# Optimization experiments

Hardware: AMD Instinct MI355X
Metric: run time of the kernel (lower is better)

Reference implementation:

```python
import jax, jax.numpy as jnp
import numpy as np

DIM = 768
HEADS = 12
HEAD_DIM = DIM // HEADS
SCALE = HEAD_DIM ** -0.5


def setup_inputs() -> dict:
    key = jax.random.key(0)
    ks = jax.random.split(key, 5)
    x = jax.random.normal(ks[0], (2, 4096, DIM), dtype=jnp.float32)
    # torch nn.Linear params: weight [out, in], bias [out]
    qkv_w = jax.random.normal(ks[1], (3 * DIM, DIM), dtype=jnp.float32) * (DIM ** -0.5)
    qkv_b = jax.random.normal(ks[2], (3 * DIM,), dtype=jnp.float32) * 0.02
    proj_w = jax.random.normal(ks[3], (DIM, DIM), dtype=jnp.float32) * (DIM ** -0.5)
    proj_b = jax.random.normal(ks[4], (DIM,), dtype=jnp.float32) * 0.02
    return {"x": x, "qkv_w": qkv_w, "qkv_b": qkv_b, "proj_w": proj_w, "proj_b": proj_b}


def reference(x, qkv_w, qkv_b, proj_w, proj_b):
    b, n, c = x.shape
    qkv = x @ qkv_w.T + qkv_b                      # [b, n, 3c]
    qkv = qkv.reshape(b, n, 3, HEADS, HEAD_DIM)
    qkv = jnp.transpose(qkv, (2, 0, 3, 1, 4))      # [3, b, h, n, d]
    q, k, v = qkv[0], qkv[1], qkv[2]
    attn = jax.nn.softmax(jnp.einsum('bhqd,bhkd->bhqk', q, k) * SCALE, axis=-1)
    out = jnp.einsum('bhqk,bhkd->bhqd', attn, v)   # [b, h, n, d]
    out = jnp.transpose(out, (0, 2, 1, 3)).reshape(b, n, c)
    return out @ proj_w.T + proj_b
```

## Files before the change

### kernel.cpp

```cpp
#include <hip/hip_runtime.h>
#include <stdint.h>

#define SEQ   4096
#define NDIM  768
#define HD    64
#define NH    12
#define NBH   24
#define MTOT  8192

#define PSTR 72

typedef short s8v __attribute__((ext_vector_type(8)));
typedef float f4v __attribute__((ext_vector_type(4)));
typedef float f16x __attribute__((ext_vector_type(16)));
typedef unsigned short u16;
typedef u16 u16x4 __attribute__((ext_vector_type(4)));
typedef uint32_t u32x4v __attribute__((ext_vector_type(4)));
typedef int i32x2 __attribute__((ext_vector_type(2)));

#define C1 0.18033688011112042f

__device__ __forceinline__ u16 f2bf(float f) {
  union { float f; uint32_t u; } cv; cv.f = f;
  const uint32_t u = cv.u;
  return (u16)((u + 0x7fffu + ((u >> 16) & 1u)) >> 16);
}
__device__ __forceinline__ float ex2(float x) { return __builtin_amdgcn_exp2f(x); }

__device__ __forceinline__ uint32_t cvtpk_bf16(float lo, float hi) {
  uint32_t r;
  asm("v_cvt_pk_bf16_f32 %0, %1, %2" : "=v"(r) : "v"(lo), "v"(hi));
  return r;
}
__device__ __forceinline__ void pl32swap(uint32_t& a, uint32_t& b) {
  i32x2 r = __builtin_amdgcn_permlane32_swap((int)a, (int)b, false, false);
  a = (uint32_t)r.x; b = (uint32_t)r.y;
}
__device__ __forceinline__ void gload_lds16(const void* g, void* l) {
  __builtin_amdgcn_global_load_lds(
      (const __attribute__((address_space(1))) uint32_t*)g,
      (__attribute__((address_space(3))) uint32_t*)l, 16, 0, 0);
}

__global__ __launch_bounds__(256) void cvt3_kernel(
    const float* __restrict__ a, u16* __restrict__ da, int na4,
    const float* __restrict__ b, u16* __restrict__ db, int nb4,
    const float* __restrict__ c, u16* __restrict__ dc, int nc4) {
  int i = blockIdx.x * 256 + threadIdx.x;
  const float* s; u16* d;
  if (i < na4)             { s = a; d = da; }
  else if (i < na4 + nb4)  { s = b; d = db; i -= na4; }
  else if (i < na4 + nb4 + nc4) { s = c; d = dc; i -= na4 + nb4; }
  else return;
  const float4 f = ((const float4*)s)[i];
  u16x4 r;
  r[0] = f2bf(f.x); r[1] = f2bf(f.y); r[2] = f2bf(f.z); r[3] = f2bf(f.w);
  ((u16x4*)d)[i] = r;
}

__global__ __launch_bounds__(256) void gemm_qkv(const u16* __restrict__ A,
    const u16* __restrict__ B, const float* __restrict__ bias,
    u16* __restrict__ qg, u16* __restrict__ kg, u16* __restrict__ vtg) {
  __shared__ __align__(16) u16 at[128 * 32];
  __shared__ __align__(16) u16 bt[128 * 32];
  const int tid  = threadIdx.x;
  const int lane = tid & 63;
  const int w    = tid >> 6;
  const int quad = lane >> 4;
  const int col  = lane & 15;
  const int m0 = blockIdx.y * 128;
  const int n0 = blockIdx.x * 128;
  const int srow = tid >> 2;
  const int schk = ((tid & 3) ^ (srow & 3)) * 8;
  const int wm = (w >> 1) * 64;
  const int wn = (w & 1) * 64;
  const int xq = (quad ^ (col & 3)) * 8;

  const f4v fz = {0.f, 0.f, 0.f, 0.f};
  f4v acc[4][4];
#pragma unroll
  for (int i = 0; i < 4; i++)
#pragma unroll
    for (int j = 0; j < 4; j++) acc[i][j] = fz;

  const u16* ga0 = A + (size_t)(m0 + srow) * NDIM + schk;
  const u16* ga1 = A + (size_t)(m0 + 64 + srow) * NDIM + schk;
  const u16* gb0 = B + (size_t)(n0 + srow) * NDIM + schk;
  const u16* gb1 = B + (size_t)(n0 + 64 + srow) * NDIM + schk;
  u16* const la = at + (size_t)w * 512;
  u16* const lb = bt + (size_t)w * 512;

  for (int k0 = 0; k0 < NDIM; k0 += 32) {
    __syncthreads();
    gload_lds16(ga0 + k0, la);
    gload_lds16(ga1 + k0, la + 2048);
    gload_lds16(gb0 + k0, lb);
    gload_lds16(gb1 + k0, lb + 2048);
    __syncthreads();
    s8v af[4], bf[4];
#pragma unroll
    for (int i = 0; i < 4; i++)
      af[i] = *(const s8v*)(at + (wm + i * 16 + col) * 32 + xq);
#pragma unroll
    for (int j = 0; j < 4; j++)
      bf[j] = *(const s8v*)(bt + (wn + j * 16 + col) * 32 + xq);
#pragma unroll
    for (int i = 0; i < 4; i++)
#pragma unroll
      for (int j = 0; j < 4; j++)
        acc[i][j] = __builtin_amdgcn_mfma_f32_16x16x32_bf16(af[i], bf[j], acc[i][j], 0, 0, 0);
  }

  const int wmg = m0 + wm;
  const int wng = n0 + wn;
  const int s = n0 / NDIM;
#pragma unroll
  for (int j = 0; j < 4; j++) {
    const int c = wng + j * 16 + col;
    const float bv = bias[c];
    const int r = c - s * NDIM;
    const int h = r >> 6;
    const int d = r & 63;
#pragma unroll
    for (int i = 0; i < 4; i++) {
      const int mb = wmg + i * 16 + quad * 4;
      const int bb = mb >> 12;
      const int n  = mb & 4095;
      const size_t hb = (size_t)(bb * NH + h);
      const f4v v = acc[i][j];
      if (s == 2) {
        u16x4 pk;
#pragma unroll
        for (int rg = 0; rg < 4; rg++) pk[rg] = f2bf(v[rg] + bv);
        *(u16x4*)(vtg + (hb * HD + d) * SEQ + n) = pk;
      } else if (s == 0) {
#pragma unroll
        for (int rg = 0; rg < 4; rg++)
          qg[(hb * SEQ + (size_t)(n + rg)) * HD + d] = f2bf((v[rg] + bv) * C1);
      } else {
#pragma unroll
        for (int rg = 0; rg < 4; rg++)
          kg[(hb * SEQ + (size_t)(n + rg)) * HD + d] = f2bf(v[rg] + bv);
      }
    }
  }
}

__global__ __launch_bounds__(256, 3) void attn_kernel(const u16* __restrict__ qg,
    const u16* __restrict__ kg, const u16* __restrict__ vtg, u16* __restrict__ og) {
  __shared__ __align__(16) u16 kls[2][64 * PSTR];
  __shared__ __align__(16) u16 vls[2][64 * PSTR];
  __shared__ float lws[4][32];

  const int tid  = threadIdx.x;
  const int lane = tid & 63;
  const int w    = tid >> 6;
  const int hi   = lane >> 5;
  const int c    = lane & 31;
  const int blk = blockIdx.x;
  const int bh  = blk % NBH;
  const int q0  = (blk / NBH) * 128;
  const size_t gbase = (size_t)bh * (SEQ * HD);
  const int wq = w * 32;

  s8v qf[4];
#pragma unroll
  for (int s = 0; s < 4; s++)
    qf[s] = *(const s8v*)(qg + gbase + (size_t)(q0 + wq + c) * HD + s * 16 + hi * 8);

  f16x o0, o1;
#pragma unroll
  for (int e = 0; e < 16; e++) { o0[e] = 0.f; o1[e] = 0.f; }
  float l0 = 0.f, l1 = 0.f, l2 = 0.f, l3 = 0.f;

  const int srow8 = tid >> 3;
  const int sch8  = (tid & 7) * 8;
  const u16* kp = kg  + gbase + (size_t)srow8 * HD  + sch8;
  const u16* vp = vtg + gbase + (size_t)srow8 * SEQ;

  s8v kr0 = *(const s8v*)(kp);
  s8v kr1 = *(const s8v*)(kp + (size_t)32 * HD);
  s8v vr0 = *(const s8v*)(vp + sch8);
  s8v vr1 = *(const s8v*)(vp + (size_t)32 * SEQ + sch8);
  *(s8v*)(kls[0] + srow8 * PSTR + sch8) = kr0;
  *(s8v*)(kls[0] + (32 + srow8) * PSTR + sch8) = kr1;
  *(s8v*)(vls[0] + srow8 * PSTR + sch8) = vr0;
  *(s8v*)(vls[0] + (32 + srow8) * PSTR + sch8) = vr1;

  for (int kb = 0; kb < SEQ; kb += 64) {
    const int cur = (kb >> 6) & 1;
    const u16* kt_ = kls[cur];
    const u16* vt_ = vls[cur];
    __syncthreads();

    if (kb + 64 < SEQ) {
      kr0 = *(const s8v*)(kp + (size_t)(kb + 64) * HD);
      kr1 = *(const s8v*)(kp + (size_t)(kb + 96) * HD);
      vr0 = *(const s8v*)(vp + kb + 64 + sch8);
      vr1 = *(const s8v*)(vp + (size_t)32 * SEQ + kb + 64 + sch8);
    }

    f16x st0, st1;
#pragma unroll
    for (int e = 0; e < 16; e++) { st0[e] = 0.f; st1[e] = 0.f; }
    __builtin_amdgcn_s_setprio(1);
#pragma unroll
    for (int s = 0; s < 4; s++) {
      const s8v k0 = *(const s8v*)(kt_ + c * PSTR + s * 16 + hi * 8);
      const s8v k1 = *(const s8v*)(kt_ + (32 + c) * PSTR + s * 16 + hi * 8);
      st0 = __builtin_amdgcn_mfma_f32_32x32x16_bf16(k0, qf[s], st0, 0, 0, 0);
      st1 = __builtin_amdgcn_mfma_f32_32x32x16_bf16(k1, qf[s], st1, 0, 0, 0);
    }
    __builtin_amdgcn_s_setprio(0);

    s8v pa0, pa1, pa2, pa3;
    {
      float p[16];
#pragma unroll
      for (int e = 0; e < 16; e++) p[e] = ex2(st0[e]);
      l0 += p[0] + p[4] + p[8]  + p[12];
      l1 += p[1] + p[5] + p[9]  + p[13];
      l2 += p[2] + p[6] + p[10] + p[14];
      l3 += p[3] + p[7] + p[11] + p[15];
      uint32_t k0 = cvtpk_bf16(p[0],  p[1]);
      uint32_t k1 = cvtpk_bf16(p[2],  p[3]);
      uint32_t k2 = cvtpk_bf16(p[4],  p[5]);
      uint32_t k3 = cvtpk_bf16(p[6],  p[7]);
      uint32_t k4 = cvtpk_bf16(p[8],  p[9]);
      uint32_t k5 = cvtpk_bf16(p[10], p[11]);
      uint32_t k6 = cvtpk_bf16(p[12], p[13]);
      uint32_t k7 = cvtpk_bf16(p[14], p[15]);
      pl32swap(k0, k2); pl32swap(k1, k3);
      pl32swap(k4, k6); pl32swap(k5, k7);
      u32x4v wA = {k0, k1, k2, k3};
      u32x4v wB = {k4, k5, k6, k7};
      pa0 = __builtin_bit_cast(s8v, wA);
      pa1 = __builtin_bit_cast(s8v, wB);
    }

    __builtin_amdgcn_s_setprio(1);
    {
      const s8v v00 = *(const s8v*)(vt_ + c * PSTR + hi * 8);
      const s8v v01 = *(const s8v*)(vt_ + (32 + c) * PSTR + hi * 8);
      const s8v v10 = *(const s8v*)(vt_ + c * PSTR + 16 + hi * 8);
      const s8v v11 = *(const s8v*)(vt_ + (32 + c) * PSTR + 16 + hi * 8);
      o0 = __builtin_amdgcn_mfma_f32_32x32x16_bf16(pa0, v00, o0, 0, 0, 0);
      o1 = __builtin_amdgcn_mfma_f32_32x32x16_bf16(pa0, v01, o1, 0, 0, 0);
      o0 = __builtin_amdgcn_mfma_f32_32x32x16_bf16(pa1, v10, o0, 0, 0, 0);
      o1 = __builtin_amdgcn_mfma_f32_32x32x16_bf16(pa1, v11, o1, 0, 0, 0);
    }
    __builtin_amdgcn_s_setprio(0);

    {
      float p[16];
#pragma unroll
      for (int e = 0; e < 16; e++) p[e] = ex2(st1[e]);
      l0 += p[0] + p[4] + p[8]  + p[12];
      l1 += p[1] + p[5] + p[9]  + p[13];
      l2 += p[2] + p[6] + p[10] + p[14];
      l3 += p[3] + p[7] + p[11] + p[15];
      uint32_t k0 = cvtpk_bf16(p[0],  p[1]);
      uint32_t k1 = cvtpk_bf16(p[2],  p[3]);
      uint32_t k2 = cvtpk_bf16(p[4],  p[5]);
      uint32_t k3 = cvtpk_bf16(p[6],  p[7]);
      uint32_t k4 = cvtpk_bf16(p[8],  p[9]);
      uint32_t k5 = cvtpk_bf16(p[10], p[11]);
      uint32_t k6 = cvtpk_bf16(p[12], p[13]);
      uint32_t k7 = cvtpk_bf16(p[14], p[15]);
      pl32swap(k0, k2); pl32swap(k1, k3);
      pl32swap(k4, k6); pl32swap(k5, k7);
      u32x4v wA = {k0, k1, k2, k3};
      u32x4v wB = {k4, k5, k6, k7};
      pa2 = __builtin_bit_cast(s8v, wA);
      pa3 = __builtin_bit_cast(s8v, wB);
    }

    if (kb + 64 < SEQ) {
      u16* kn = (u16*)kls[cur ^ 1];
      u16* vn = (u16*)vls[cur ^ 1];
      *(s8v*)(kn + srow8 * PSTR + sch8) = kr0;
      *(s8v*)(kn + (32 + srow8) * PSTR + sch8) = kr1;
      *(s8v*)(vn + srow8 * PSTR + sch8) = vr0;
      *(s8v*)(vn + (32 + srow8) * PSTR + sch8) = vr1;
    }

    __builtin_amdgcn_s_setprio(1);
    {
      const s8v v20 = *(const s8v*)(vt_ + c * PSTR + 32 + hi * 8);
      const s8v v21 = *(const s8v*)(vt_ + (32 + c) * PSTR + 32 + hi * 8);
      const s8v v30 = *(const s8v*)(vt_ + c * PSTR + 48 + hi * 8);
      const s8v v31 = *(const s8v*)(vt_ + (32 + c) * PSTR + 48 + hi * 8);
      o0 = __builtin_amdgcn_mfma_f32_32x32x16_bf16(pa2, v20, o0, 0, 0, 0);
      o1 = __builtin_amdgcn_mfma_f32_32x32x16_bf16(pa2, v21, o1, 0, 0, 0);
      o0 = __builtin_amdgcn_mfma_f32_32x32x16_bf16(pa3, v30, o0, 0, 0, 0);
      o1 = __builtin_amdgcn_mfma_f32_32x32x16_bf16(pa3, v31, o1, 0, 0, 0);
    }
    __builtin_amdgcn_s_setprio(0);
  }

  float lt = l0 + l1 + l2 + l3;
  lt += __shfl_xor(lt, 32);
  const float inv = 1.0f / lt;
  if (hi == 0) lws[w][c] = inv;

  const int b = bh / NH;
  const int h = bh % NH;
  u16* obase = og + (size_t)(b * SEQ + q0 + wq) * NDIM + h * HD + c;
#pragma unroll
  for (int r = 0; r < 16; r++) {
    const int row = (r & 3) + 8 * (r >> 2) + 4 * hi;
    const float invr = lws[w][row];
    u16* rp = obase + (size_t)row * NDIM;
    rp[0]  = f2bf(o0[r] * invr);
    rp[32] = f2bf(o1[r] * invr);
  }
}

__global__ __launch_bounds__(256) void gemm_proj(const u16* __restrict__ A,
    const u16* __restrict__ B, const float* __restrict__ bias, float* __restrict__ out) {
  __shared__ __align__(16) u16 at[128 * 32];
  __shared__ __align__(16) u16 bt[128 * 32];
  const int tid  = threadIdx.x;
  const int lane = tid & 63;
  const int w    = tid >> 6;
  const int quad = lane >> 4;
  const int col  = lane & 15;
  const int m0 = blockIdx.y * 128;
  const int n0 = blockIdx.x * 128;
  const int srow = tid >> 2;
  const int schk = ((tid & 3) ^ (srow & 3)) * 8;
  const int wm = (w >> 1) * 64;
  const int wn = (w & 1) * 64;
  const int xq = (quad ^ (col & 3)) * 8;

  const f4v fz = {0.f, 0.f, 0.f, 0.f};
  f4v acc[4][4];
#pragma unroll
  for (int i = 0; i < 4; i++)
#pragma unroll
    for (int j = 0; j < 4; j++) acc[i][j] = fz;

  const u16* ga0 = A + (size_t)(m0 + srow) * NDIM + schk;
  const u16* ga1 = A + (size_t)(m0 + 64 + srow) * NDIM + schk;
  const u16* gb0 = B + (size_t)(n0 + srow) * NDIM + schk;
  const u16* gb1 = B + (size_t)(n0 + 64 + srow) * NDIM + schk;
  u16* const la = at + (size_t)w * 512;
  u16* const lb = bt + (size_t)w * 512;

  for (int k0 = 0; k0 < NDIM; k0 += 32) {
    __syncthreads();
    gload_lds16(ga0 + k0, la);
    gload_lds16(ga1 + k0, la + 2048);
    gload_lds16(gb0 + k0, lb);
    gload_lds16(gb1 + k0, lb + 2048);
    __syncthreads();
    s8v af[4], bf[4];
#pragma unroll
    for (int i = 0; i < 4; i++)
      af[i] = *(const s8v*)(at + (wm + i * 16 + col) * 32 + xq);
#pragma unroll
    for (int j = 0; j < 4; j++)
      bf[j] = *(const s8v*)(bt + (wn + j * 16 + col) * 32 + xq);
#pragma unroll
    for (int i = 0; i < 4; i++)
#pragma unroll
      for (int j = 0; j < 4; j++)
        acc[i][j] = __builtin_amdgcn_mfma_f32_16x16x32_bf16(af[i], bf[j], acc[i][j], 0, 0, 0);
  }

  const int wmg = m0 + wm;
  const int wng = n0 + wn;
#pragma unroll
  for (int j = 0; j < 4; j++) {
    const int c = wng + j * 16 + col;
    const float bv = bias[c];
#pragma unroll
    for (int i = 0; i < 4; i++) {
#pragma unroll
      for (int rg = 0; rg < 4; rg++)
        out[(size_t)(wmg + i * 16 + quad * 4 + rg) * NDIM + c] = acc[i][j][rg] + bv;
    }
  }
}

extern "C" void kernel_launch(void* const* d_in, const int* in_sizes, int n_in,
                              void* d_out, int out_size, void* d_ws, size_t ws_size,
                              hipStream_t stream) {
  const float* x      = (const float*)d_in[0];
  const float* qkv_w  = (const float*)d_in[1];
  const float* qkv_b  = (const float*)d_in[2];
  const float* proj_w = (const float*)d_in[3];
  const float* proj_b = (const float*)d_in[4];
  float* out = (float*)d_out;

  u16* ws   = (u16*)d_ws;
  u16* x_bf = ws;
  u16* wq   = x_bf + (size_t)MTOT * NDIM;
  u16* wp   = wq + (size_t)3 * NDIM * NDIM;
  u16* q_bf = wp + (size_t)NDIM * NDIM;
  u16* k_bf = q_bf + (size_t)NBH * SEQ * HD;
  u16* vt   = k_bf + (size_t)NBH * SEQ * HD;
  u16* a_bf = vt + (size_t)NBH * SEQ * HD;

  const int nx = MTOT * NDIM / 4, nw1 = 3 * NDIM * NDIM / 4, nw2 = NDIM * NDIM / 4;
  const int ntot = nx + nw1 + nw2;
  cvt3_kernel<<<(ntot + 255) / 256, 256, 0, stream>>>(x, x_bf, nx, qkv_w, wq, nw1,
                                                      proj_w, wp, nw2);

  gemm_qkv<<<dim3(18, 64), 256, 0, stream>>>(x_bf, wq, qkv_b, q_bf, k_bf, vt);
  attn_kernel<<<768, 256, 0, stream>>>(q_bf, k_bf, vt, a_bf);
  gemm_proj<<<dim3(6, 64), 256, 0, stream>>>(a_bf, wp, proj_b, out);
}
```

Before: 278.8 us.

## Split attention key tile across wave pairs with swizzled LDS and direct loads

Restructures the attention kernel so each pair of waves owns 64 query rows and each wave in the pair handles half of every 64-key tile. The two partial outputs and row sums are then combined through shared memory at the end. The padded K/V shared tiles are replaced by an XOR-swizzled layout filled by direct global-to-LDS loads, removing the register staging and explicit shared-memory stores. V fragments are reused across two query sub-tiles, and the occupancy hint drops from 3 to 2 blocks. The costs are more accumulator registers per wave and an extra cross-wave reduction at the end.

```diff
diff --git a/kernel.cpp b/kernel.cpp
--- a/kernel.cpp
+++ b/kernel.cpp
@@ -7,8 +7,6 @@
 #define NH    12
 #define NBH   24
 #define MTOT  8192
-
-#define PSTR 72
 
 typedef short s8v __attribute__((ext_vector_type(8)));
 typedef float f4v __attribute__((ext_vector_type(4)));
@@ -146,82 +144,100 @@
   }
 }
 
-__global__ __launch_bounds__(256, 3) void attn_kernel(const u16* __restrict__ qg,
+__global__ __launch_bounds__(256, 2) void attn_kernel(const u16* __restrict__ qg,
     const u16* __restrict__ kg, const u16* __restrict__ vtg, u16* __restrict__ og) {
-  __shared__ __align__(16) u16 kls[2][64 * PSTR];
-  __shared__ __align__(16) u16 vls[2][64 * PSTR];
-  __shared__ float lws[4][32];
+  __shared__ __align__(16) u16 smem[2][2][4096];
+  __shared__ float lred[2][64];
 
   const int tid  = threadIdx.x;
   const int lane = tid & 63;
   const int w    = tid >> 6;
   const int hi   = lane >> 5;
   const int c    = lane & 31;
+  const int kth  = w & 1;
+  const int pair = w >> 1;
   const int blk = blockIdx.x;
   const int bh  = blk % NBH;
   const int q0  = (blk / NBH) * 128;
   const size_t gbase = (size_t)bh * (SEQ * HD);
-  const int wq = w * 32;
-
-  s8v qf[4];
-#pragma unroll
-  for (int s = 0; s < 4; s++)
-    qf[s] = *(const s8v*)(qg + gbase + (size_t)(q0 + wq + c) * HD + s * 16 + hi * 8);
-
-  f16x o0, o1;
-#pragma unroll
-  for (int e = 0; e < 16; e++) { o0[e] = 0.f; o1[e] = 0.f; }
-  float l0 = 0.f, l1 = 0.f, l2 = 0.f, l3 = 0.f;
-
-  const int srow8 = tid >> 3;
-  const int sch8  = (tid & 7) * 8;
-  const u16* kp = kg  + gbase + (size_t)srow8 * HD  + sch8;
-  const u16* vp = vtg + gbase + (size_t)srow8 * SEQ;
-
-  s8v kr0 = *(const s8v*)(kp);
-  s8v kr1 = *(const s8v*)(kp + (size_t)32 * HD);
-  s8v vr0 = *(const s8v*)(vp + sch8);
-  s8v vr1 = *(const s8v*)(vp + (size_t)32 * SEQ + sch8);
-  *(s8v*)(kls[0] + srow8 * PSTR + sch8) = kr0;
-  *(s8v*)(kls[0] + (32 + srow8) * PSTR + sch8) = kr1;
-  *(s8v*)(vls[0] + srow8 * PSTR + sch8) = vr0;
-  *(s8v*)(vls[0] + (32 + srow8) * PSTR + sch8) = vr1;
+  const int qw = pair * 64;
+
+  s8v qfA[4], qfB[4];
+#pragma unroll
+  for (int s = 0; s < 4; s++) {
+    qfA[s] = *(const s8v*)(qg + gbase + (size_t)(q0 + qw + c) * HD + s * 16 + hi * 8);
+    qfB[s] = *(const s8v*)(qg + gbase + (size_t)(q0 + qw + 32 + c) * HD + s * 16 + hi * 8);
+  }
+
+  f16x zacc;
+#pragma unroll
+  for (int e = 0; e < 16; e++) zacc[e] = 0.f;
+  f16x o00 = zacc, o01 = zacc, o10 = zacc, o11 = zacc;
+  float l0a = 0.f, l1a = 0.f, l2a = 0.f, l3a = 0.f;
+  float l0b = 0.f, l1b = 0.f, l2b = 0.f, l3b = 0.f;
+
+  const int lrow  = lane >> 3;
+  const int lslot = (lane & 7) ^ lrow;
+  const u16* kgl0 = kg  + gbase + (size_t)(w * 16 + lrow) * HD  + lslot * 8;
+  const u16* kgl1 = kgl0 + (size_t)8 * HD;
+  const u16* vgl0 = vtg + gbase + (size_t)(w * 16 + lrow) * SEQ + lslot * 8;
+  const u16* vgl1 = vgl0 + (size_t)8 * SEQ;
+
+  {
+    u16* kd = (u16*)smem[0][0] + w * 1024;
+    u16* vd = (u16*)smem[0][1] + w * 1024;
+    gload_lds16(kgl0, kd);
+    gload_lds16(kgl1, kd + 512);
+    gload_lds16(vgl0, vd);
+    gload_lds16(vgl1, vd + 512);
+  }
+
+  const int kbase = kth * 2048 + c * 64;
+  const int c7 = c & 7;
 
   for (int kb = 0; kb < SEQ; kb += 64) {
     const int cur = (kb >> 6) & 1;
-    const u16* kt_ = kls[cur];
-    const u16* vt_ = vls[cur];
+    const u16* kb_ = smem[cur][0];
+    const u16* vb_ = smem[cur][1];
     __syncthreads();
 
     if (kb + 64 < SEQ) {
-      kr0 = *(const s8v*)(kp + (size_t)(kb + 64) * HD);
-      kr1 = *(const s8v*)(kp + (size_t)(kb + 96) * HD);
-      vr0 = *(const s8v*)(vp + kb + 64 + sch8);
-      vr1 = *(const s8v*)(vp + (size_t)32 * SEQ + kb + 64 + sch8);
-    }
-
-    f16x st0, st1;
-#pragma unroll
-    for (int e = 0; e < 16; e++) { st0[e] = 0.f; st1[e] = 0.f; }
+      const int nb = cur ^ 1;
+      u16* kd = (u16*)smem[nb][0] + w * 1024;
+      u16* vd = (u16*)smem[nb][1] + w * 1024;
+      gload_lds16(kgl0 + (size_t)(kb + 64) * HD, kd);
+      gload_lds16(kgl1 + (size_t)(kb + 64) * HD, kd + 512);
+      gload_lds16(vgl0 + (kb + 64), vd);
+      gload_lds16(vgl1 + (kb + 64), vd + 512);
+    }
+
     __builtin_amdgcn_s_setprio(1);
-#pragma unroll
-    for (int s = 0; s < 4; s++) {
-      const s8v k0 = *(const s8v*)(kt_ + c * PSTR + s * 16 + hi * 8);
-      const s8v k1 = *(const s8v*)(kt_ + (32 + c) * PSTR + s * 16 + hi * 8);
-      st0 = __builtin_amdgcn_mfma_f32_32x32x16_bf16(k0, qf[s], st0, 0, 0, 0);
-      st1 = __builtin_amdgcn_mfma_f32_32x32x16_bf16(k1, qf[s], st1, 0, 0, 0);
+    f16x sA, sB;
+    {
+      const s8v kf0 = *(const s8v*)(kb_ + kbase + ((((0 * 2 + hi)) ^ c7) << 3));
+      sA = __builtin_amdgcn_mfma_f32_32x32x16_bf16(kf0, qfA[0], zacc, 0, 0, 0);
+      sB = __builtin_amdgcn_mfma_f32_32x32x16_bf16(kf0, qfB[0], zacc, 0, 0, 0);
+      const s8v kf1 = *(const s8v*)(kb_ + kbase + ((((1 * 2 + hi)) ^ c7) << 3));
+      sA = __builtin_amdgcn_mfma_f32_32x32x16_bf16(kf1, qfA[1], sA, 0, 0, 0);
+      sB = __builtin_amdgcn_mfma_f32_32x32x16_bf16(kf1, qfB[1], sB, 0, 0, 0);
+      const s8v kf2 = *(const s8v*)(kb_ + kbase + ((((2 * 2 + hi)) ^ c7) << 3));
+      sA = __builtin_amdgcn_mfma_f32_32x32x16_bf16(kf2, qfA[2], sA, 0, 0, 0);
+      sB = __builtin_amdgcn_mfma_f32_32x32x16_bf16(kf2, qfB[2], sB, 0, 0, 0);
+      const s8v kf3 = *(const s8v*)(kb_ + kbase + ((((3 * 2 + hi)) ^ c7) << 3));
+      sA = __builtin_amdgcn_mfma_f32_32x32x16_bf16(kf3, qfA[3], sA, 0, 0, 0);
+      sB = __builtin_amdgcn_mfma_f32_32x32x16_bf16(kf3, qfB[3], sB, 0, 0, 0);
     }
     __builtin_amdgcn_s_setprio(0);
 
-    s8v pa0, pa1, pa2, pa3;
+    s8v pa00, pa01, pa10, pa11;
     {
       float p[16];
 #pragma unroll
-      for (int e = 0; e < 16; e++) p[e] = ex2(st0[e]);
-      l0 += p[0] + p[4] + p[8]  + p[12];
-      l1 += p[1] + p[5] + p[9]  + p[13];
-      l2 += p[2] + p[6] + p[10] + p[14];
-      l3 += p[3] + p[7] + p[11] + p[15];
+      for (int e = 0; e < 16; e++) p[e] = ex2(sA[e]);
+      l0a += p[0] + p[4] + p[8]  + p[12];
+      l1a += p[1] + p[5] + p[9]  + p[13];
+      l2a += p[2] + p[6] + p[10] + p[14];
+      l3a += p[3] + p[7] + p[11] + p[15];
       uint32_t k0 = cvtpk_bf16(p[0],  p[1]);
       uint32_t k1 = cvtpk_bf16(p[2],  p[3]);
       uint32_t k2 = cvtpk_bf16(p[4],  p[5]);
@@ -234,31 +250,32 @@
       pl32swap(k4, k6); pl32swap(k5, k7);
       u32x4v wA = {k0, k1, k2, k3};
       u32x4v wB = {k4, k5, k6, k7};
-      pa0 = __builtin_bit_cast(s8v, wA);
-      pa1 = __builtin_bit_cast(s8v, wB);
-    }
-
+      pa00 = __builtin_bit_cast(s8v, wA);
+      pa01 = __builtin_bit_cast(s8v, wB);
+    }
+
+    s8v vf0, vf1, vf2, vf3;
     __builtin_amdgcn_s_setprio(1);
     {
-      const s8v v00 = *(const s8v*)(vt_ + c * PSTR + hi * 8);
-      const s8v v01 = *(const s8v*)(vt_ + (32 + c) * PSTR + hi * 8);
-      const s8v v10 = *(const s8v*)(vt_ + c * PSTR + 16 + hi * 8);
-      const s8v v11 = *(const s8v*)(vt_ + (32 + c) * PSTR + 16 + hi * 8);
-      o0 = __builtin_amdgcn_mfma_f32_32x32x16_bf16(pa0, v00, o0, 0, 0, 0);
-      o1 = __builtin_amdgcn_mfma_f32_32x32x16_bf16(pa0, v01, o1, 0, 0, 0);
-      o0 = __builtin_amdgcn_mfma_f32_32x32x16_bf16(pa1, v10, o0, 0, 0, 0);
-      o1 = __builtin_amdgcn_mfma_f32_32x32x16_bf16(pa1, v11, o1, 0, 0, 0);
+      vf0 = *(const s8v*)(vb_ + 0 * 2048 + c * 64 + (((kth * 4 + 0 + hi) ^ c7) << 3));
+      vf1 = *(const s8v*)(vb_ + 1 * 2048 + c * 64 + (((kth * 4 + 0 + hi) ^ c7) << 3));
+      vf2 = *(const s8v*)(vb_ + 0 * 2048 + c * 64 + (((kth * 4 + 2 + hi) ^ c7) << 3));
+      vf3 = *(const s8v*)(vb_ + 1 * 2048 + c * 64 + (((kth * 4 + 2 + hi) ^ c7) << 3));
+      o00 = __builtin_amdgcn_mfma_f32_32x32x16_bf16(pa00, vf0, o00, 0, 0, 0);
+      o01 = __builtin_amdgcn_mfma_f32_32x32x16_bf16(pa00, vf1, o01, 0, 0, 0);
+      o00 = __builtin_amdgcn_mfma_f32_32x32x16_bf16(pa01, vf2, o00, 0, 0, 0);
+      o01 = __builtin_amdgcn_mfma_f32_32x32x16_bf16(pa01, vf3, o01, 0, 0, 0);
     }
     __builtin_amdgcn_s_setprio(0);
 
     {
       float p[16];
 #pragma unroll
-      for (int e = 0; e < 16; e++) p[e] = ex2(st1[e]);
-      l0 += p[0] + p[4] + p[8]  + p[12];
-      l1 += p[1] + p[5] + p[9]  + p[13];
-      l2 += p[2] + p[6] + p[10] + p[14];
-      l3 += p[3] + p[7] + p[11] + p[15];
+      for (int e = 0; e < 16; e++) p[e] = ex2(sB[e]);
+      l0b += p[0] + p[4] + p[8]  + p[12];
+      l1b += p[1] + p[5] + p[9]  + p[13];
+      l2b += p[2] + p[6] + p[10] + p[14];
+      l3b += p[3] + p[7] + p[11] + p[15];
       uint32_t k0 = cvtpk_bf16(p[0],  p[1]);
       uint32_t k1 = cvtpk_bf16(p[2],  p[3]);
       uint32_t k2 = cvtpk_bf16(p[4],  p[5]);
@@ -271,48 +288,56 @@
       pl32swap(k4, k6); pl32swap(k5, k7);
       u32x4v wA = {k0, k1, k2, k3};
       u32x4v wB = {k4, k5, k6, k7};
-      pa2 = __builtin_bit_cast(s8v, wA);
-      pa3 = __builtin_bit_cast(s8v, wB);
-    }
-
-    if (kb + 64 < SEQ) {
-      u16* kn = (u16*)kls[cur ^ 1];
-      u16* vn = (u16*)vls[cur ^ 1];
-      *(s8v*)(kn + srow8 * PSTR + sch8) = kr0;
-      *(s8v*)(kn + (32 + srow8) * PSTR + sch8) = kr1;
-      *(s8v*)(vn + srow8 * PSTR + sch8) = vr0;
-      *(s8v*)(vn + (32 + srow8) * PSTR + sch8) = vr1;
+      pa10 = __builtin_bit_cast(s8v, wA);
+      pa11 = __builtin_bit_cast(s8v, wB);
     }
 
     __builtin_amdgcn_s_setprio(1);
     {
-      const s8v v20 = *(const s8v*)(vt_ + c * PSTR + 32 + hi * 8);
-      const s8v v21 = *(const s8v*)(vt_ + (32 + c) * PSTR + 32 + hi * 8);
-      const s8v v30 = *(const s8v*)(vt_ + c * PSTR + 48 + hi * 8);
-      const s8v v31 = *(const s8v*)(vt_ + (32 + c) * PSTR + 48 + hi * 8);
-      o0 = __builtin_amdgcn_mfma_f32_32x32x16_bf16(pa2, v20, o0, 0, 0, 0);
-      o1 = __builtin_amdgcn_mfma_f32_32x32x16_bf16(pa2, v21, o1, 0, 0, 0);
-      o0 = __builtin_amdgcn_mfma_f32_32x32x16_bf16(pa3, v30, o0, 0, 0, 0);
-      o1 = __builtin_amdgcn_mfma_f32_32x32x16_bf16(pa3, v31, o1, 0, 0, 0);
+      o10 = __builtin_amdgcn_mfma_f32_32x32x16_bf16(pa10, vf0, o10, 0, 0, 0);
+      o11 = __builtin_amdgcn_mfma_f32_32x32x16_bf16(pa10, vf1, o11, 0, 0, 0);
+      o10 = __builtin_amdgcn_mfma_f32_32x32x16_bf16(pa11, vf2, o10, 0, 0, 0);
+      o11 = __builtin_amdgcn_mfma_f32_32x32x16_bf16(pa11, vf3, o11, 0, 0, 0);
     }
     __builtin_amdgcn_s_setprio(0);
   }
 
-  float lt = l0 + l1 + l2 + l3;
-  lt += __shfl_xor(lt, 32);
-  const float inv = 1.0f / lt;
-  if (hi == 0) lws[w][c] = inv;
-
-  const int b = bh / NH;
-  const int h = bh % NH;
-  u16* obase = og + (size_t)(b * SEQ + q0 + wq) * NDIM + h * HD + c;
-#pragma unroll
-  for (int r = 0; r < 16; r++) {
-    const int row = (r & 3) + 8 * (r >> 2) + 4 * hi;
-    const float invr = lws[w][row];
-    u16* rp = obase + (size_t)row * NDIM;
-    rp[0]  = f2bf(o0[r] * invr);
-    rp[32] = f2bf(o1[r] * invr);
+  float* M  = (float*)smem + pair * 4096;
+  float* LP = lred[pair];
+  float ltA = l0a + l1a + l2a + l3a;  ltA += __shfl_xor(ltA, 32);
+  float ltB = l0b + l1b + l2b + l3b;  ltB += __shfl_xor(ltB, 32);
+  __syncthreads();
+  if (kth) {
+    if (hi == 0) { LP[c] = ltA; LP[32 + c] = ltB; }
+#pragma unroll
+    for (int r = 0; r < 16; r++) {
+      const int rq = (r & 3) + 8 * (r >> 2) + 4 * hi;
+      M[rq * 64 + c]             = o00[r];
+      M[rq * 64 + 32 + c]        = o01[r];
+      M[(32 + rq) * 64 + c]      = o10[r];
+      M[(32 + rq) * 64 + 32 + c] = o11[r];
+    }
+  }
+  __syncthreads();
+  if (!kth) {
+    const float invA = 1.0f / (ltA + LP[c]);
+    const float invB = 1.0f / (ltB + LP[32 + c]);
+    if (hi == 0) { LP[c] = invA; LP[32 + c] = invB; }
+    const int b = bh / NH;
+    const int h = bh % NH;
+    u16* obase = og + (size_t)(b * SEQ + q0 + pair * 64) * NDIM + h * HD;
+#pragma unroll
+    for (int r = 0; r < 16; r++) {
+      const int rq = (r & 3) + 8 * (r >> 2) + 4 * hi;
+      const float iA = LP[rq];
+      const float iB = LP[32 + rq];
+      u16* r0 = obase + (size_t)rq * NDIM;
+      u16* r1 = obase + (size_t)(32 + rq) * NDIM;
+      r0[c]      = f2bf((o00[r] + M[rq * 64 + c]) * iA);
+      r0[32 + c] = f2bf((o01[r] + M[rq * 64 + 32 + c]) * iA);
+      r1[c]      = f2bf((o10[r] + M[(32 + rq) * 64 + c]) * iB);
+      r1[32 + c] = f2bf((o11[r] + M[(32 + rq) * 64 + 32 + c]) * iB);
+    }
   }
 }
 
```

Measured after the change: 302.9 us. +8.6%, slower.

## Store Q transposed with packed writes and remap GEMM blocks across XCDs

Applied to the files above, without the earlier changes.

The QKV GEMM epilogue now writes Q in a transposed [bh, d, n] layout using packed 4-element stores, in place of scattered 2-byte stores. The attention kernel reads its Q fragments from that layout with strided scalar loads. Both GEMMs move to a 1D grid whose block-to-tile mapping groups consecutive tiles onto the same XCD (bid&7), aiming for better L2 locality on the MI355X chiplets. The cost is that the Q loads in attention become 32 strided 2-byte reads per lane, though these happen only once per block.

```diff
diff --git a/kernel.cpp b/kernel.cpp
--- a/kernel.cpp
+++ b/kernel.cpp
@@ -60,7 +60,7 @@
 
 __global__ __launch_bounds__(256) void gemm_qkv(const u16* __restrict__ A,
     const u16* __restrict__ B, const float* __restrict__ bias,
-    u16* __restrict__ qg, u16* __restrict__ kg, u16* __restrict__ vtg) {
+    u16* __restrict__ qtg, u16* __restrict__ kg, u16* __restrict__ vtg) {
   __shared__ __align__(16) u16 at[128 * 32];
   __shared__ __align__(16) u16 bt[128 * 32];
   const int tid  = threadIdx.x;
@@ -68,8 +68,10 @@
   const int w    = tid >> 6;
   const int quad = lane >> 4;
   const int col  = lane & 15;
-  const int m0 = blockIdx.y * 128;
-  const int n0 = blockIdx.x * 128;
+  const int bid  = blockIdx.x;
+  const int wgid = (bid & 7) * 144 + (bid >> 3);
+  const int n0 = (wgid % 18) * 128;
+  const int m0 = (wgid / 18) * 128;
   const int srow = tid >> 2;
   const int schk = ((tid & 3) ^ (srow & 3)) * 8;
   const int wm = (w >> 1) * 64;
@@ -134,9 +136,10 @@
         for (int rg = 0; rg < 4; rg++) pk[rg] = f2bf(v[rg] + bv);
         *(u16x4*)(vtg + (hb * HD + d) * SEQ + n) = pk;
       } else if (s == 0) {
-#pragma unroll
-        for (int rg = 0; rg < 4; rg++)
-          qg[(hb * SEQ + (size_t)(n + rg)) * HD + d] = f2bf((v[rg] + bv) * C1);
+        u16x4 pk;
+#pragma unroll
+        for (int rg = 0; rg < 4; rg++) pk[rg] = f2bf((v[rg] + bv) * C1);
+        *(u16x4*)(qtg + (hb * HD + d) * SEQ + n) = pk;
       } else {
 #pragma unroll
         for (int rg = 0; rg < 4; rg++)
@@ -146,7 +149,7 @@
   }
 }
 
-__global__ __launch_bounds__(256, 3) void attn_kernel(const u16* __restrict__ qg,
+__global__ __launch_bounds__(256, 3) void attn_kernel(const u16* __restrict__ qtg,
     const u16* __restrict__ kg, const u16* __restrict__ vtg, u16* __restrict__ og) {
   __shared__ __align__(16) u16 kls[2][64 * PSTR];
   __shared__ __align__(16) u16 vls[2][64 * PSTR];
@@ -164,9 +167,17 @@
   const int wq = w * 32;
 
   s8v qf[4];
-#pragma unroll
-  for (int s = 0; s < 4; s++)
-    qf[s] = *(const s8v*)(qg + gbase + (size_t)(q0 + wq + c) * HD + s * 16 + hi * 8);
+  {
+    const u16* qp = qtg + gbase + (q0 + wq + c);
+#pragma unroll
+    for (int s = 0; s < 4; s++) {
+      s8v t;
+#pragma unroll
+      for (int j = 0; j < 8; j++)
+        t[j] = (short)qp[(size_t)(s * 16 + hi * 8 + j) * SEQ];
+      qf[s] = t;
+    }
+  }
 
   f16x o0, o1;
 #pragma unroll
@@ -325,8 +336,10 @@
   const int w    = tid >> 6;
   const int quad = lane >> 4;
   const int col  = lane & 15;
-  const int m0 = blockIdx.y * 128;
-  const int n0 = blockIdx.x * 128;
+  const int bid  = blockIdx.x;
+  const int wgid = (bid & 7) * 48 + (bid >> 3);
+  const int n0 = (wgid % 6) * 128;
+  const int m0 = (wgid / 6) * 128;
   const int srow = tid >> 2;
   const int schk = ((tid & 3) ^ (srow & 3)) * 8;
   const int wm = (w >> 1) * 64;
@@ -397,8 +410,8 @@
   u16* x_bf = ws;
   u16* wq   = x_bf + (size_t)MTOT * NDIM;
   u16* wp   = wq + (size_t)3 * NDIM * NDIM;
-  u16* q_bf = wp + (size_t)NDIM * NDIM;
-  u16* k_bf = q_bf + (size_t)NBH * SEQ * HD;
+  u16* qt   = wp + (size_t)NDIM * NDIM;
+  u16* k_bf = qt + (size_t)NBH * SEQ * HD;
   u16* vt   = k_bf + (size_t)NBH * SEQ * HD;
   u16* a_bf = vt + (size_t)NBH * SEQ * HD;
 
@@ -407,7 +420,7 @@
   cvt3_kernel<<<(ntot + 255) / 256, 256, 0, stream>>>(x, x_bf, nx, qkv_w, wq, nw1,
                                                       proj_w, wp, nw2);
 
-  gemm_qkv<<<dim3(18, 64), 256, 0, stream>>>(x_bf, wq, qkv_b, q_bf, k_bf, vt);
-  attn_kernel<<<768, 256, 0, stream>>>(q_bf, k_bf, vt, a_bf);
-  gemm_proj<<<dim3(6, 64), 256, 0, stream>>>(a_bf, wp, proj_b, out);
-}
+  gemm_qkv<<<1152, 256, 0, stream>>>(x_bf, wq, qkv_b, qt, k_bf, vt);
+  attn_kernel<<<768, 256, 0, stream>>>(qt, k_bf, vt, a_bf);
+  gemm_proj<<<384, 256, 0, stream>>>(a_bf, wp, proj_b, out);
+}
```

Measured after the change: 271.8 us. 1.03x faster.
